# Optimization experiments

Measured on AMD Instinct MI355X. Metric: run time of the kernel, lower is better.

Reference implementation:

```python
import jax, jax.numpy as jnp
import numpy as np

N_ENT, N_REL, RANK = 40943, 11, 256
IMG_DIM, LING_DIM = 1000, 768
BATCH = 1000
ALPHA, GAMMA, SCALE = 0.1, 0.8, 100.0
REG, SINKHORN_ITERS, NUM_OT = 0.05, 100, 10


def _sinkhorn_plan(mm_row, st_row):
    """Entropic-OT plan between uniform marginals over mm_dim and st_dim.
    Cost (as in cal_ot): ((st[:,None]-mm[None,:])**2 * scale).T -> [mm_dim, st_dim].
    Log-domain Sinkhorn for stability. Returns plan of shape [mm_dim, st_dim]."""
    mm_dim, st_dim = mm_row.shape[0], st_row.shape[0]
    M = ((st_row[:, None] - mm_row[None, :]) ** 2 * SCALE).T  # [mm_dim, st_dim]
    logK = -M / REG
    loga = -jnp.log(jnp.float32(mm_dim))  # uniform marginal log-prob
    logb = -jnp.log(jnp.float32(st_dim))
    f0 = jnp.zeros((mm_dim,), M.dtype)
    g0 = jnp.zeros((st_dim,), M.dtype)

    def body(i, fg):
        f, g = fg
        f = REG * (loga - jax.nn.logsumexp(logK + g[None, :] / REG, axis=1))
        g = REG * (logb - jax.nn.logsumexp(logK + f[:, None] / REG, axis=0))
        return (f, g)

    f, g = jax.lax.fori_loop(0, SINKHORN_ITERS, body, (f0, g0))
    return jnp.exp(logK + (f[:, None] + g[None, :]) / REG)


def _cal_ot(mm_vec, st_emb, delta_ot):
    # torch code runs this under no_grad -> stop_gradient on the OT part.
    plans = jax.vmap(_sinkhorn_plan)(mm_vec[:NUM_OT], st_emb[:NUM_OT])  # [10, mm_dim, st_dim]
    st_dim = st_emb.shape[-1]
    return jax.lax.stop_gradient(plans.mean(axis=0) * st_dim * SCALE) + delta_ot


def setup_inputs() -> dict:
    key = jax.random.key(0)
    ks = jax.random.split(key, 9)
    heads = jax.random.randint(ks[0], (BATCH,), 0, N_ENT)
    rels = jax.random.randint(ks[1], (BATCH,), 0, N_REL)
    tails = jax.random.randint(ks[2], (BATCH,), 0, N_ENT)
    x = jnp.stack([heads, rels, tails], axis=1).astype(jnp.int64)
    emb_ent = jax.random.normal(ks[3], (N_ENT, 2 * RANK), jnp.float32) * 0.001
    emb_rel = jax.random.normal(ks[4], (N_REL, 2 * RANK), jnp.float32) * 0.001
    xav_img = float(np.sqrt(2.0 / (IMG_DIM + 2 * RANK)))
    xav_ling = float(np.sqrt(2.0 / (LING_DIM + 2 * RANK)))
    mats_img = jax.random.normal(ks[5], (IMG_DIM, 2 * RANK), jnp.float32) * xav_img
    mats_ling = jax.random.normal(ks[6], (LING_DIM, 2 * RANK), jnp.float32) * xav_ling
    img_vec = jax.random.normal(ks[7], (N_ENT, IMG_DIM), jnp.float32)
    ling_vec = jax.random.normal(ks[8], (N_ENT, LING_DIM), jnp.float32)
    return {"x": x, "emb_ent": emb_ent, "emb_rel": emb_rel, "mats_img": mats_img,
            "mats_ling": mats_ling, "img_vec": img_vec, "ling_vec": ling_vec}


def reference(x, emb_ent, emb_rel, mats_img, mats_ling, img_vec, ling_vec):
    matrix1 = _cal_ot(img_vec, emb_ent, mats_img)    # [img_dim, 2r]
    matrix2 = _cal_ot(ling_vec, emb_ent, mats_ling)  # [ling_dim, 2r]
    img_embeddings = img_vec @ matrix1               # [n_ent, 2r]
    ling_embeddings = ling_vec @ matrix2             # [n_ent, 2r]
    embedding = (1.0 - ALPHA - GAMMA) * emb_ent + ALPHA * img_embeddings + GAMMA * ling_embeddings

    lhs = embedding[x[:, 0]]  # [B, 2r]
    rel = emb_rel[x[:, 1]]
    rhs = embedding[x[:, 2]]
    l0, l1 = lhs[:, :RANK], lhs[:, RANK:]
    r0, r1 = rel[:, :RANK], rel[:, RANK:]
    h0, h1 = rhs[:, :RANK], rhs[:, RANK:]
    t0, t1 = embedding[:, :RANK], embedding[:, RANK:]

    scores = (l0 * r0 - l1 * r1) @ t0.T + (l0 * r1 + l1 * r0) @ t1.T  # [B, n_ent]
    factors = (jnp.sqrt(l0 ** 2 + l1 ** 2),
               jnp.sqrt(r0 ** 2 + r1 ** 2),
               jnp.sqrt(h0 ** 2 + h1 ** 2))
    return scores, factors
```

## Files before the change

### kernel.cpp

```cpp
#include <hip/hip_runtime.h>

#define NENT 40943

typedef short bf16x8 __attribute__((ext_vector_type(8)));
typedef float f32x4 __attribute__((ext_vector_type(4)));
typedef unsigned long long u64;

__device__ __forceinline__ unsigned short f2bf(float f) {
  unsigned int u = __builtin_bit_cast(unsigned int, f);
  u += 0x7fffu + ((u >> 16) & 1u);
  return (unsigned short)(u >> 16);
}
__device__ __forceinline__ float bf2f(unsigned short h) {
  unsigned int u = ((unsigned int)h) << 16;
  return __builtin_bit_cast(float, u);
}

#define K2C 2885.3900817779268f

__device__ __forceinline__ float tval(u64 v) {
  return __builtin_bit_cast(float, (unsigned int)(v & 0xffffffffu));
}
__device__ __forceinline__ float tagged_poll(const u64* p, unsigned int tag) {
  u64 v;
  for (;;) {
    v = __hip_atomic_load(p, __ATOMIC_RELAXED, __HIP_MEMORY_SCOPE_AGENT);
    if ((unsigned int)(v >> 32) >= tag) break;
    __builtin_amdgcn_s_sleep(1);
  }
  return tval(v);
}
__device__ __forceinline__ void tagged_store(u64* p, unsigned int tag, float f) {
  u64 v = ((u64)tag << 32) | (u64)__builtin_bit_cast(unsigned int, f);
  __hip_atomic_store(p, v, __ATOMIC_RELAXED, __HIP_MEMORY_SCOPE_AGENT);
}

__global__ void init_k(const float* __restrict__ emb_ent, const float* __restrict__ img,
                       const float* __restrict__ ling, u64* __restrict__ phiT,
                       u64* __restrict__ gamT, float* __restrict__ A2, float* __restrict__ B2,
                       float* __restrict__ C2) {
  const int p = blockIdx.x, t = threadIdx.x;
  const int pm = p % 10;
  const bool isImg = (p < 10);
  const int D = isImg ? 1000 : 768;
  const float* st = emb_ent + (size_t)pm * 512;
  const float* mm = isImg ? (img + (size_t)pm * 1000) : (ling + (size_t)pm * 768);
  for (int s = t; s < 512; s += 256) {
    float sv = st[s];
    A2[p * 512 + s] = -K2C * sv * sv;
    B2[p * 512 + s] = 2.f * K2C * sv;
    gamT[p * 512 + s] = 0ull;
  }
  for (int m = t; m < 1024; m += 256) {
    float c2 = 0.f;
    if (m < D) { float mv = mm[m]; c2 = -K2C * mv * mv; }
    C2[p * 1024 + m] = c2;
    phiT[p * 1024 + m] = 0ull;
  }
}

__global__ __launch_bounds__(512) void sinkhorn_k(
    const float* __restrict__ img, const float* __restrict__ ling,
    u64* __restrict__ phiT, u64* __restrict__ gamT,
    const float* __restrict__ A2, const float* __restrict__ B2,
    const float* __restrict__ C2) {
  const int bid = blockIdx.x;
  const int p = bid / 12, j = bid % 12;
  const int pm = p % 10;
  const bool isImg = (p < 10);
  const int D = isImg ? 1000 : 768;
  const float* mm = isImg ? (img + (size_t)pm * 1000) : (ling + (size_t)pm * 768);
  u64* phiP = phiT + p * 1024;
  u64* gamP = gamT + p * 512;
  const float* A2P = A2 + p * 512;
  const float* B2P = B2 + p * 512;
  const float* C2P = C2 + p * 1024;
  const float negLog2D = isImg ? -9.965784284662087f : -9.584962500721156f;

  const int TPMF = isImg ? 6 : 8;
  const int fChunk = isImg ? 84 : 64;
  const int fm0 = j * fChunk;
  int fCount = D - fm0; if (fCount > fChunk) fCount = fChunk;
  const int gs0 = j * 43;
  int gCount = 512 - gs0; if (gCount > 43) gCount = 43;

  __shared__ float2 wb[512];
  __shared__ float2 um[1024];
  __shared__ float redM[512];
  __shared__ float redA[512];

  const int t = threadIdx.x;
  wb[t].y = B2P[t];
  for (int m = t; m < D; m += 512) um[m].y = mm[m];
  const float wbA2 = A2P[t];

  const int fml = t / TPMF, fq = t - fml * TPMF;
  const bool fAct = (fml < fCount);
  const int fs0 = (fq * 512) / TPMF, fs1 = ((fq + 1) * 512) / TPMF;
  const int fmG = fm0 + fml;
  float fmm = 0.f, fC2 = 0.f;
  if (fAct) { fmm = mm[fmG]; fC2 = C2P[fmG]; }

  const int TPMG = 11;
  const int gsl = t / TPMG, gq = t - gsl * TPMG;
  const bool gAct = (gsl < gCount);
  const int gm0 = (gq * D) / TPMG, gm1 = ((gq + 1) * D) / TPMG;
  const int gsG = gs0 + gsl;
  float gA2 = 0.f;
  if (gAct) gA2 = A2P[gsG];

  for (int it = 0; it < 100; ++it) {
    const unsigned int gtag = 2u * (unsigned)it;
    const unsigned int ptag = 2u * (unsigned)it + 1u;

    wb[t].x = wbA2 + tagged_poll(&gamP[t], gtag);
    __syncthreads();
    if (fAct) {
      float vmax = -3.0e38f;
      for (int s = fs0; s < fs1; ++s) {
        float2 w = wb[s];
        vmax = fmaxf(vmax, fmaf(w.y, fmm, w.x));
      }
      float acc = 0.f;
      for (int s = fs0; s < fs1; ++s) {
        float2 w = wb[s];
        acc += __builtin_exp2f(fmaf(w.y, fmm, w.x) - vmax);
      }
      redM[t] = vmax; redA[t] = acc;
    }
    __syncthreads();
    if (fAct && fq == 0) {
      float vmax = redM[t], acc = redA[t];
      for (int q = 1; q < TPMF; ++q) {
        float m2 = redM[t + q], a2 = redA[t + q];
        float M = fmaxf(vmax, m2);
        acc = acc * __builtin_exp2f(vmax - M) + a2 * __builtin_exp2f(m2 - M);
        vmax = M;
      }
      tagged_store(&phiP[fmG], ptag, negLog2D - fC2 - vmax - __builtin_log2f(acc));
    }

    for (int m = t; m < D; m += 512) um[m].x = C2P[m] + tagged_poll(&phiP[m], ptag);
    __syncthreads();
    if (gAct) {
      float bs = wb[gsG].y;
      float vmax = -3.0e38f;
      for (int m = gm0; m < gm1; ++m) {
        float2 u = um[m];
        vmax = fmaxf(vmax, fmaf(u.y, bs, u.x));
      }
      float acc = 0.f;
      for (int m = gm0; m < gm1; ++m) {
        float2 u = um[m];
        acc += __builtin_exp2f(fmaf(u.y, bs, u.x) - vmax);
      }
      redM[t] = vmax; redA[t] = acc;
    }
    __syncthreads();
    if (gAct && gq == 0) {
      float vmax = redM[t], acc = redA[t];
      for (int q = 1; q < TPMG; ++q) {
        float m2 = redM[t + q], a2 = redA[t + q];
        float M = fmaxf(vmax, m2);
        acc = acc * __builtin_exp2f(vmax - M) + a2 * __builtin_exp2f(m2 - M);
        vmax = M;
      }
      tagged_store(&gamP[gsG], gtag + 2u, -9.0f - gA2 - vmax - __builtin_log2f(acc));
    }
    __syncthreads();
  }
}

__global__ void build_b(const float* __restrict__ mats_img, const float* __restrict__ mats_ling,
                        const float* __restrict__ img, const float* __restrict__ ling,
                        const u64* __restrict__ phiT, const u64* __restrict__ gamT,
                        const float* __restrict__ A2, const float* __restrict__ B2,
                        const float* __restrict__ C2, unsigned short* __restrict__ BbigT) {
  const int k = blockIdx.x, t = threadIdx.x;
  if (k >= 1768) {
    for (int n = t; n < 512; n += 256) BbigT[(size_t)n * 1792 + k] = 0;
    return;
  }
  const bool isImg = (k < 1000);
  const int kk = isImg ? k : (k - 1000);
  __shared__ float sU[10], sMM[10];
  if (t < 10) {
    const int p = isImg ? t : (10 + t);
    sU[t] = C2[p * 1024 + kk] + tval(phiT[p * 1024 + kk]);
    sMM[t] = isImg ? img[(size_t)t * 1000 + kk] : ling[(size_t)t * 768 + kk];
  }
  __syncthreads();
  const float* mats = isImg ? mats_img : mats_ling;
  const float scale = isImg ? 0.1f : 0.8f;
  const int pbase = isImg ? 0 : 10;
  for (int n = t; n < 512; n += 256) {
    float val = 0.f;
    #pragma unroll
    for (int i = 0; i < 10; ++i) {
      const int p = pbase + i;
      float a = A2[p * 512 + n] + tval(gamT[p * 512 + n]);
      float b = B2[p * 512 + n];
      val += __builtin_exp2f(fmaf(b, sMM[i], a + sU[i]));
    }
    float outv = scale * fmaf(5120.f, val, mats[(size_t)kk * 512 + n]);
    BbigT[(size_t)n * 1792 + k] = f2bf(outv);
  }
}

__global__ __launch_bounds__(256) void gemm1_k(
    const float* __restrict__ img, const float* __restrict__ ling,
    const float* __restrict__ emb_ent, const unsigned short* __restrict__ BbigT,
    unsigned short* __restrict__ Eb) {
  const int bid0 = blockIdx.x;
  const int wg = (bid0 & 7) * 160 + (bid0 >> 3);
  const int nt = wg & 3, mt = wg >> 2;
  const int m0 = mt * 128, n0 = nt * 128;
  __shared__ __align__(16) unsigned short As[128 * 40];
  __shared__ __align__(16) unsigned short Bs[128 * 40];
  const int t = threadIdx.x;
  const int wave = t >> 6, lane = t & 63;
  const int quad = lane >> 4, lrow = lane & 15;
  const int wm = (wave & 1) * 64, wn = (wave >> 1) * 64;
  f32x4 acc[4][4];
  #pragma unroll
  for (int a = 0; a < 4; ++a)
    #pragma unroll
    for (int b = 0; b < 4; ++b) acc[a][b] = (f32x4){0.f, 0.f, 0.f, 0.f};

  const int r = t >> 1, h = t & 1;
  const int gm = m0 + r;
  const bool mOK = (gm < NENT);
  const float* arowI = img + (size_t)gm * 1000;
  const float* arowL = ling + (size_t)gm * 768;
  const unsigned short* brow = BbigT + (size_t)(n0 + r) * 1792;
  unsigned short* asDst = As + r * 40 + h * 16;
  unsigned short* bsDst = Bs + r * 40 + h * 16;

  for (int k0 = 0; k0 < 1792; k0 += 32) {
    const int ck = k0 + h * 16;
    unsigned short u[16];
    #pragma unroll
    for (int q4 = 0; q4 < 4; ++q4) {
      const int kk = ck + q4 * 4;
      f32x4 v = (f32x4){0.f, 0.f, 0.f, 0.f};
      if (mOK) {
        if (kk < 1000) v = *(const f32x4*)(arowI + kk);
        else if (kk < 1768) v = *(const f32x4*)(arowL + (kk - 1000));
      }
      u[q4 * 4 + 0] = f2bf(v.x); u[q4 * 4 + 1] = f2bf(v.y);
      u[q4 * 4 + 2] = f2bf(v.z); u[q4 * 4 + 3] = f2bf(v.w);
    }
    bf16x8 w0, w1;
    #pragma unroll
    for (int i2 = 0; i2 < 8; ++i2) { w0[i2] = (short)u[i2]; w1[i2] = (short)u[8 + i2]; }
    *(bf16x8*)asDst = w0;
    *(bf16x8*)(asDst + 8) = w1;
    bf16x8 b0 = *(const bf16x8*)(brow + ck);
    bf16x8 b1 = *(const bf16x8*)(brow + ck + 8);
    *(bf16x8*)bsDst = b0;
    *(bf16x8*)(bsDst + 8) = b1;
    __syncthreads();
    bf16x8 af[4], bfv[4];
    #pragma unroll
    for (int i2 = 0; i2 < 4; ++i2) {
      af[i2] = *(const bf16x8*)(As + (wm + i2 * 16 + lrow) * 40 + quad * 8);
      bfv[i2] = *(const bf16x8*)(Bs + (wn + i2 * 16 + lrow) * 40 + quad * 8);
    }
    #pragma unroll
    for (int mi = 0; mi < 4; ++mi)
      #pragma unroll
      for (int ni = 0; ni < 4; ++ni)
        acc[mi][ni] = __builtin_amdgcn_mfma_f32_16x16x32_bf16(af[mi], bfv[ni], acc[mi][ni], 0, 0, 0);
    __syncthreads();
  }
  #pragma unroll
  for (int mi = 0; mi < 4; ++mi) {
    const int mbase = m0 + wm + mi * 16 + quad * 4;
    #pragma unroll
    for (int ni = 0; ni < 4; ++ni) {
      const int n = n0 + wn + ni * 16 + lrow;
      #pragma unroll
      for (int rr = 0; rr < 4; ++rr) {
        const int gm2 = mbase + rr;
        if (gm2 < NENT) {
          float v = acc[mi][ni][rr] + 0.1f * emb_ent[(size_t)gm2 * 512 + n];
          Eb[(size_t)gm2 * 512 + n] = f2bf(v);
        }
      }
    }
  }
}

__global__ void gather_c(const int* __restrict__ x, const unsigned short* __restrict__ Eb,
                         const float* __restrict__ emb_rel, unsigned short* __restrict__ cb,
                         float* __restrict__ outF) {
  const int i = blockIdx.x, t = threadIdx.x;
  if (i >= 1000) {
    cb[(size_t)i * 512 + t] = 0;
    cb[(size_t)i * 512 + 256 + t] = 0;
    return;
  }
  const int hI = x[i * 3 + 0], rI = x[i * 3 + 1], tI = x[i * 3 + 2];
  const float l0 = bf2f(Eb[(size_t)hI * 512 + t]);
  const float l1 = bf2f(Eb[(size_t)hI * 512 + 256 + t]);
  const float r0 = emb_rel[(size_t)rI * 512 + t];
  const float r1 = emb_rel[(size_t)rI * 512 + 256 + t];
  const float h0 = bf2f(Eb[(size_t)tI * 512 + t]);
  const float h1 = bf2f(Eb[(size_t)tI * 512 + 256 + t]);
  cb[(size_t)i * 512 + t] = f2bf(l0 * r0 - l1 * r1);
  cb[(size_t)i * 512 + 256 + t] = f2bf(l0 * r1 + l1 * r0);
  outF[(size_t)i * 256 + t] = sqrtf(l0 * l0 + l1 * l1);
  outF[256000 + (size_t)i * 256 + t] = sqrtf(r0 * r0 + r1 * r1);
  outF[512000 + (size_t)i * 256 + t] = sqrtf(h0 * h0 + h1 * h1);
}

__global__ __launch_bounds__(256) void gemm2_k(
    const unsigned short* __restrict__ cb, const unsigned short* __restrict__ Eb,
    float* __restrict__ scores) {
  const int bid0 = blockIdx.x;
  const int wg = (bid0 & 7) * 320 + (bid0 >> 3);
  const int mt = wg & 7, nt = wg >> 3;
  const int m0 = mt * 128, n0 = nt * 128;
  __shared__ __align__(16) unsigned short As[128 * 40];
  __shared__ __align__(16) unsigned short Bs[128 * 40];
  const int t = threadIdx.x;
  const int wave = t >> 6, lane = t & 63;
  const int quad = lane >> 4, lrow = lane & 15;
  const int wm = (wave & 1) * 64, wn = (wave >> 1) * 64;
  f32x4 acc[4][4];
  #pragma unroll
  for (int a = 0; a < 4; ++a)
    #pragma unroll
    for (int b = 0; b < 4; ++b) acc[a][b] = (f32x4){0.f, 0.f, 0.f, 0.f};

  const int r = t >> 1, h = t & 1;
  const unsigned short* arow = cb + (size_t)(m0 + r) * 512;
  const int ge = n0 + r;
  const bool nOK = (ge < NENT);
  const unsigned short* browE = Eb + (size_t)ge * 512;
  unsigned short* asDst = As + r * 40 + h * 16;
  unsigned short* bsDst = Bs + r * 40 + h * 16;

  for (int k0 = 0; k0 < 512; k0 += 32) {
    const int ck = k0 + h * 16;
    bf16x8 a0 = *(const bf16x8*)(arow + ck);
    bf16x8 a1 = *(const bf16x8*)(arow + ck + 8);
    *(bf16x8*)asDst = a0;
    *(bf16x8*)(asDst + 8) = a1;
    bf16x8 b0 = (bf16x8)0, b1 = (bf16x8)0;
    if (nOK) { b0 = *(const bf16x8*)(browE + ck); b1 = *(const bf16x8*)(browE + ck + 8); }
    *(bf16x8*)bsDst = b0;
    *(bf16x8*)(bsDst + 8) = b1;
    __syncthreads();
    bf16x8 af[4], bfv[4];
    #pragma unroll
    for (int i2 = 0; i2 < 4; ++i2) {
      af[i2] = *(const bf16x8*)(As + (wm + i2 * 16 + lrow) * 40 + quad * 8);
      bfv[i2] = *(const bf16x8*)(Bs + (wn + i2 * 16 + lrow) * 40 + quad * 8);
    }
    #pragma unroll
    for (int mi = 0; mi < 4; ++mi)
      #pragma unroll
      for (int ni = 0; ni < 4; ++ni)
        acc[mi][ni] = __builtin_amdgcn_mfma_f32_16x16x32_bf16(af[mi], bfv[ni], acc[mi][ni], 0, 0, 0);
    __syncthreads();
  }
  #pragma unroll
  for (int mi = 0; mi < 4; ++mi) {
    const int mbase = m0 + wm + mi * 16 + quad * 4;
    #pragma unroll
    for (int ni = 0; ni < 4; ++ni) {
      const int n = n0 + wn + ni * 16 + lrow;
      if (n < NENT) {
        #pragma unroll
        for (int rr = 0; rr < 4; ++rr) {
          const int i = mbase + rr;
          if (i < 1000) scores[(size_t)i * NENT + n] = acc[mi][ni][rr];
        }
      }
    }
  }
}

extern "C" void kernel_launch(void* const* d_in, const int* in_sizes, int n_in,
                              void* d_out, int out_size, void* d_ws, size_t ws_size,
                              hipStream_t stream) {
  (void)in_sizes; (void)n_in; (void)out_size; (void)ws_size;
  const int*   x        = (const int*)d_in[0];
  const float* emb_ent  = (const float*)d_in[1];
  const float* emb_rel  = (const float*)d_in[2];
  const float* mats_img = (const float*)d_in[3];
  const float* mats_ling= (const float*)d_in[4];
  const float* img_vec  = (const float*)d_in[5];
  const float* ling_vec = (const float*)d_in[6];
  float* out = (float*)d_out;

  u64* phiT = (u64*)d_ws;
  u64* gamT = phiT + 20 * 1024;
  float* A2  = (float*)(gamT + 20 * 512);
  float* B2  = A2 + 20 * 512;
  float* C2  = B2 + 20 * 512;
  unsigned short* BbigT = (unsigned short*)(C2 + 20 * 1024);
  unsigned short* Eb = BbigT + (size_t)512 * 1792;
  unsigned short* cb = Eb + (size_t)NENT * 512;

  init_k<<<dim3(20), dim3(256), 0, stream>>>(emb_ent, img_vec, ling_vec, phiT, gamT, A2, B2, C2);
  sinkhorn_k<<<dim3(240), dim3(512), 0, stream>>>(img_vec, ling_vec, phiT, gamT, A2, B2, C2);
  build_b<<<dim3(1792), dim3(256), 0, stream>>>(mats_img, mats_ling, img_vec, ling_vec,
                                                phiT, gamT, A2, B2, C2, BbigT);
  gemm1_k<<<dim3(1280), dim3(256), 0, stream>>>(img_vec, ling_vec, emb_ent, BbigT, Eb);
  gather_c<<<dim3(1024), dim3(256), 0, stream>>>(x, Eb, emb_rel, cb, out + (size_t)1000 * NENT);
  gemm2_k<<<dim3(2560), dim3(256), 0, stream>>>(cb, Eb, out);
}
```

Baseline: 3.163 ms.

## Add Sinkhorn convergence early-exit and widen blocks to 1024 threads

Each Sinkhorn block now records how much every potential changed since the previous iteration. It leaves the loop once no potential moved by more than a tiny epsilon. All blocks of a problem read the same global potentials, so they should decide to exit on the same iteration. Block size goes from 512 to 1024 threads, doubling the lanes per row and column in the logsumexp reductions, and the reduction loops are fully unrolled into register arrays. The aim is to cut the serial per-iteration latency and skip iterations after convergence. In exchange it adds an extra barrier per iteration, raises register pressure, and makes results depend on the epsilon threshold.

```diff
diff --git a/kernel.cpp b/kernel.cpp
--- a/kernel.cpp
+++ b/kernel.cpp
@@ -17,6 +17,8 @@
 }
 
 #define K2C 2885.3900817779268f
+#define NEGB (-3.0e38f)
+#define CONV_EPS 5.9604644775390625e-08f
 
 __device__ __forceinline__ float tval(u64 v) {
   return __builtin_bit_cast(float, (unsigned int)(v & 0xffffffffu));
@@ -59,7 +61,7 @@
   }
 }
 
-__global__ __launch_bounds__(512) void sinkhorn_k(
+__global__ __launch_bounds__(1024, 4) void sinkhorn_k(
     const float* __restrict__ img, const float* __restrict__ ling,
     u64* __restrict__ phiT, u64* __restrict__ gamT,
     const float* __restrict__ A2, const float* __restrict__ B2,
@@ -77,22 +79,26 @@
   const float* C2P = C2 + p * 1024;
   const float negLog2D = isImg ? -9.965784284662087f : -9.584962500721156f;
 
-  const int TPMF = isImg ? 6 : 8;
+  const int TPMF = isImg ? 12 : 16;
   const int fChunk = isImg ? 84 : 64;
   const int fm0 = j * fChunk;
   int fCount = D - fm0; if (fCount > fChunk) fCount = fChunk;
   const int gs0 = j * 43;
   int gCount = 512 - gs0; if (gCount > 43) gCount = 43;
+  const int TPMG = 23;
 
   __shared__ float2 wb[512];
   __shared__ float2 um[1024];
-  __shared__ float redM[512];
-  __shared__ float redA[512];
+  __shared__ float redM[1024];
+  __shared__ float redA[1024];
+  __shared__ int sFbad[2], sGbad[2];
 
   const int t = threadIdx.x;
-  wb[t].y = B2P[t];
-  for (int m = t; m < D; m += 512) um[m].y = mm[m];
-  const float wbA2 = A2P[t];
+  if (t < 512) wb[t].y = B2P[t];
+  for (int m = t; m < D; m += 1024) um[m].y = mm[m];
+  const float wbA2 = (t < 512) ? A2P[t] : 0.f;
+  float gPrev = 0.f;
+  float pPrev = 0.f;
 
   const int fml = t / TPMF, fq = t - fml * TPMF;
   const bool fAct = (fml < fCount);
@@ -101,30 +107,53 @@
   float fmm = 0.f, fC2 = 0.f;
   if (fAct) { fmm = mm[fmG]; fC2 = C2P[fmG]; }
 
-  const int TPMG = 11;
   const int gsl = t / TPMG, gq = t - gsl * TPMG;
   const bool gAct = (gsl < gCount);
   const int gm0 = (gq * D) / TPMG, gm1 = ((gq + 1) * D) / TPMG;
   const int gsG = gs0 + gsl;
-  float gA2 = 0.f;
-  if (gAct) gA2 = A2P[gsG];
+  float gA2 = 0.f, gBs = 0.f;
+  if (gAct) { gA2 = A2P[gsG]; gBs = B2P[gsG]; }
+
+  if (t == 0) { sFbad[0] = 0; sFbad[1] = 0; sGbad[0] = 0; sGbad[1] = 0; }
+  __syncthreads();
 
   for (int it = 0; it < 100; ++it) {
     const unsigned int gtag = 2u * (unsigned)it;
     const unsigned int ptag = 2u * (unsigned)it + 1u;
-
-    wb[t].x = wbA2 + tagged_poll(&gamP[t], gtag);
-    __syncthreads();
+    const int par = it & 1;
+
+    float d = 0.f;
+    if (t < 512) {
+      float nv = tagged_poll(&gamP[t], gtag);
+      d = fabsf(nv - gPrev); gPrev = nv;
+      wb[t].x = wbA2 + nv;
+    }
+    if (__ballot(d > CONV_EPS)) { if ((t & 63) == 0) sFbad[par] = 1; }
+    __syncthreads();
+
     if (fAct) {
-      float vmax = -3.0e38f;
-      for (int s = fs0; s < fs1; ++s) {
-        float2 w = wb[s];
-        vmax = fmaxf(vmax, fmaf(w.y, fmm, w.x));
-      }
-      float acc = 0.f;
-      for (int s = fs0; s < fs1; ++s) {
-        float2 w = wb[s];
-        acc += __builtin_exp2f(fmaf(w.y, fmm, w.x) - vmax);
+      float vmax = NEGB, acc = 0.f;
+      if (isImg) {
+        float z[43];
+        #pragma unroll
+        for (int i = 0; i < 43; ++i) {
+          const int s = fs0 + i;
+          float zz = NEGB;
+          if (s < fs1) { float2 w = wb[s]; zz = fmaf(w.y, fmm, w.x); }
+          z[i] = zz; vmax = fmaxf(vmax, zz);
+        }
+        #pragma unroll
+        for (int i = 0; i < 43; ++i) acc += __builtin_exp2f(z[i] - vmax);
+      } else {
+        float z[32];
+        #pragma unroll
+        for (int i = 0; i < 32; ++i) {
+          float2 w = wb[fs0 + i];
+          float zz = fmaf(w.y, fmm, w.x);
+          z[i] = zz; vmax = fmaxf(vmax, zz);
+        }
+        #pragma unroll
+        for (int i = 0; i < 32; ++i) acc += __builtin_exp2f(z[i] - vmax);
       }
       redM[t] = vmax; redA[t] = acc;
     }
@@ -140,19 +169,39 @@
       tagged_store(&phiP[fmG], ptag, negLog2D - fC2 - vmax - __builtin_log2f(acc));
     }
 
-    for (int m = t; m < D; m += 512) um[m].x = C2P[m] + tagged_poll(&phiP[m], ptag);
-    __syncthreads();
+    float d2 = 0.f;
+    if (t < D) {
+      float nv = tagged_poll(&phiP[t], ptag);
+      d2 = fabsf(nv - pPrev); pPrev = nv;
+      um[t].x = C2P[t] + nv;
+    }
+    if (__ballot(d2 > CONV_EPS)) { if ((t & 63) == 0) sGbad[par] = 1; }
+    __syncthreads();
+
     if (gAct) {
-      float bs = wb[gsG].y;
-      float vmax = -3.0e38f;
-      for (int m = gm0; m < gm1; ++m) {
-        float2 u = um[m];
-        vmax = fmaxf(vmax, fmaf(u.y, bs, u.x));
-      }
-      float acc = 0.f;
-      for (int m = gm0; m < gm1; ++m) {
-        float2 u = um[m];
-        acc += __builtin_exp2f(fmaf(u.y, bs, u.x) - vmax);
+      float vmax = NEGB, acc = 0.f;
+      if (isImg) {
+        float z[44];
+        #pragma unroll
+        for (int i = 0; i < 44; ++i) {
+          const int m = gm0 + i;
+          float zz = NEGB;
+          if (m < gm1) { float2 u = um[m]; zz = fmaf(u.y, gBs, u.x); }
+          z[i] = zz; vmax = fmaxf(vmax, zz);
+        }
+        #pragma unroll
+        for (int i = 0; i < 44; ++i) acc += __builtin_exp2f(z[i] - vmax);
+      } else {
+        float z[34];
+        #pragma unroll
+        for (int i = 0; i < 34; ++i) {
+          const int m = gm0 + i;
+          float zz = NEGB;
+          if (m < gm1) { float2 u = um[m]; zz = fmaf(u.y, gBs, u.x); }
+          z[i] = zz; vmax = fmaxf(vmax, zz);
+        }
+        #pragma unroll
+        for (int i = 0; i < 34; ++i) acc += __builtin_exp2f(z[i] - vmax);
       }
       redM[t] = vmax; redA[t] = acc;
     }
@@ -168,6 +217,11 @@
       tagged_store(&gamP[gsG], gtag + 2u, -9.0f - gA2 - vmax - __builtin_log2f(acc));
     }
     __syncthreads();
+
+    const bool ex = (sFbad[par] | sGbad[par]) == 0;
+    if (t == 0) { sFbad[par ^ 1] = 0; sGbad[par ^ 1] = 0; }
+    __syncthreads();
+    if (ex) break;
   }
 }
 
@@ -405,7 +459,7 @@
   unsigned short* cb = Eb + (size_t)NENT * 512;
 
   init_k<<<dim3(20), dim3(256), 0, stream>>>(emb_ent, img_vec, ling_vec, phiT, gamT, A2, B2, C2);
-  sinkhorn_k<<<dim3(240), dim3(512), 0, stream>>>(img_vec, ling_vec, phiT, gamT, A2, B2, C2);
+  sinkhorn_k<<<dim3(240), dim3(1024), 0, stream>>>(img_vec, ling_vec, phiT, gamT, A2, B2, C2);
   build_b<<<dim3(1792), dim3(256), 0, stream>>>(mats_img, mats_ling, img_vec, ling_vec,
                                                 phiT, gamT, A2, B2, C2, BbigT);
   gemm1_k<<<dim3(1280), dim3(256), 0, stream>>>(img_vec, ling_vec, emb_ent, BbigT, Eb);
```

Result: no change. 3.201 ms (+1.2%).
